# Performance work log

Measured on AMD Instinct MI355X. Metric: run time of the kernel, lower is better.

## Reference

```python
import jax, jax.numpy as jnp
import numpy as np

TOPK = 13
ALPHA = 1.0
BETA = 6.0
NUM_CLASSES = 80
EPS = 1e-9


def _make_boxes(key, shape, max_half):
    # shape = (..., 4): build valid x1y1x2y2 boxes inside a 640x640 image
    kc, ks = jax.random.split(key)
    centers = jax.random.uniform(kc, shape[:-1] + (2,), minval=30.0, maxval=610.0)
    halves = jax.random.uniform(ks, shape[:-1] + (2,), minval=2.0, maxval=max_half)
    return jnp.concatenate([centers - halves, centers + halves], axis=-1)


def setup_inputs() -> dict:
    key = jax.random.key(0)
    k1, k2, k3, k4, k5 = jax.random.split(key, 5)
    B, L, C, n = 16, 8400, NUM_CLASSES, 128
    pred_scores = jax.random.uniform(k1, (B, L, C), dtype=jnp.float32)
    pred_bboxes = _make_boxes(k2, (B, L, 4), 60.0)
    anchor_points = jax.random.uniform(k3, (L, 2), minval=0.0, maxval=640.0)
    gt_labels = jax.random.randint(k4, (B, n), 0, C, dtype=jnp.int32)
    gt_bboxes = _make_boxes(k5, (B, n, 4), 120.0)
    pad_gt_mask = jnp.ones((B, n, 1), dtype=jnp.float32)
    return {"pred_scores": pred_scores, "pred_bboxes": pred_bboxes,
            "anchor_points": anchor_points, "gt_labels": gt_labels,
            "gt_bboxes": gt_bboxes, "pad_gt_mask": pad_gt_mask}


def _batch_iou(box1, box2, eps=1e-9):
    # box1: [B, n, 4], box2: [B, L, 4] -> iou [B, n, L]
    b1 = box1[:, :, None]  # [B,n,1,4]
    b2 = box2[:, None]     # [B,1,L,4]
    x1y1 = jnp.maximum(b1[..., 0:2], b2[..., 0:2])
    x2y2 = jnp.minimum(b1[..., 2:4], b2[..., 2:4])
    overlap = jnp.prod(jnp.clip(x2y2 - x1y1, 0.0), axis=-1)
    area1 = jnp.prod(jnp.clip(b1[..., 2:4] - b1[..., 0:2], 0.0), axis=-1)
    area2 = jnp.prod(jnp.clip(b2[..., 2:4] - b2[..., 0:2], 0.0), axis=-1)
    return overlap / (area1 + area2 - overlap + eps)


def _points_in_bboxes(points, bboxes, eps=EPS):
    # points: [L,2], bboxes: [B,n,4] -> [B,n,L] float
    x = points[None, None, :, 0]
    y = points[None, None, :, 1]
    xmin = bboxes[..., 0:1]; ymin = bboxes[..., 1:2]
    xmax = bboxes[..., 2:3]; ymax = bboxes[..., 3:4]
    l = x - xmin; t = y - ymin; r = xmax - x; b = ymax - y
    d = jnp.minimum(jnp.minimum(l, t), jnp.minimum(r, b))
    return (d > eps).astype(bboxes.dtype)


def _gather_topk(metrics, topk, topk_mask):
    # metrics: [B,n,L] -> one-hot membership of per-gt topk anchors [B,n,L]
    L = metrics.shape[-1]
    _, topk_idxs = jax.lax.top_k(metrics, topk)          # [B,n,topk]
    is_in_topk = jax.nn.one_hot(topk_idxs, L, dtype=metrics.dtype).sum(-2)
    return is_in_topk * topk_mask


def reference(pred_scores, pred_bboxes, anchor_points, gt_labels, gt_bboxes, pad_gt_mask):
    B, n, _ = gt_bboxes.shape
    L = pred_bboxes.shape[1]
    # pairwise IoU between gts and predicted boxes: [B,n,L]
    ious = _batch_iou(gt_bboxes, pred_bboxes)
    # per-gt class scores gathered from pred_scores: [B,n,L]
    scores_cl = jnp.transpose(pred_scores, (0, 2, 1))                 # [B,C,L]
    bbox_cls_scores = jnp.take_along_axis(scores_cl, gt_labels[:, :, None].astype(jnp.int32), axis=1)
    # task-aligned metric
    alignment = (bbox_cls_scores ** ALPHA) * (ious ** BETA)
    is_in_gts = _points_in_bboxes(anchor_points, gt_bboxes)           # [B,n,L]
    is_in_topk = _gather_topk(alignment * is_in_gts, TOPK, pad_gt_mask)
    mask_positive = is_in_topk * is_in_gts * pad_gt_mask              # [B,n,L]
    # resolve anchors assigned to multiple gts: keep max-IoU gt
    mask_pos_sum = mask_positive.sum(-2)                              # [B,L]
    is_max_iou = jnp.transpose(jax.nn.one_hot(jnp.argmax(ious, axis=-2), n, dtype=ious.dtype), (0, 2, 1))
    mask_positive = jnp.where((mask_pos_sum[:, None, :] > 1), is_max_iou, mask_positive)
    mask_pos_sum = mask_positive.sum(-2)
    # assignment
    assigned_gt_index = jnp.argmax(mask_positive, axis=-2)            # [B,L]
    flat_idx = assigned_gt_index + jnp.arange(B, dtype=assigned_gt_index.dtype)[:, None] * n
    assigned_labels = jnp.reshape(gt_labels, (-1,))[flat_idx]
    assigned_labels = jnp.where(mask_pos_sum > 0, assigned_labels, NUM_CLASSES)
    assigned_bboxes = jnp.reshape(gt_bboxes, (-1, 4))[flat_idx]       # [B,L,4]
    assigned_scores = jax.nn.one_hot(assigned_labels, NUM_CLASSES + 1, dtype=pred_scores.dtype)[..., :NUM_CLASSES]
    # rescale scores by normalized alignment metric
    align_m = alignment * mask_positive
    max_metric = align_m.max(-1, keepdims=True)                       # [B,n,1]
    max_iou = (ious * mask_positive).max(-1, keepdims=True)           # [B,n,1]
    align_m = (align_m / (max_metric + EPS)) * max_iou
    assigned_scores = assigned_scores * align_m.max(-2)[..., None]    # [B,L,C]
    return assigned_labels, assigned_bboxes, assigned_scores
```

## Files before the change

kernel.cpp:

```cpp
#include <hip/hip_runtime.h>
#include <stdint.h>

#define BB   16
#define NGT  128
#define LL   8400
#define CC   80
#define KTOP 13
#define SEGW 2112
#define FEPS 1e-9f

typedef float vfloat4 __attribute__((ext_vector_type(4)));

__device__ __forceinline__ float iou_f(float4 g, float4 p) {
    float ix0 = fmaxf(g.x, p.x);
    float iy0 = fmaxf(g.y, p.y);
    float ix1 = fminf(g.z, p.z);
    float iy1 = fminf(g.w, p.w);
    float ow = fmaxf(ix1 - ix0, 0.0f);
    float oh = fmaxf(iy1 - iy0, 0.0f);
    float ov = ow * oh;
    float a1 = fmaxf(g.z - g.x, 0.0f) * fmaxf(g.w - g.y, 0.0f);
    float a2 = fmaxf(p.z - p.x, 0.0f) * fmaxf(p.w - p.y, 0.0f);
    return ov / (a1 + a2 - ov + FEPS);
}

__global__ __launch_bounds__(256) void topk_kernel(
    const float*  __restrict__ pred_scores,
    const float4* __restrict__ pred_bboxes,
    const float2* __restrict__ anchors,
    const int*    __restrict__ gt_labels,
    const float4* __restrict__ gt_bboxes,
    int* __restrict__ claim_count,
    int* __restrict__ claimant)
{
    int wave = threadIdx.x >> 6;
    int lane = threadIdx.x & 63;
    int row  = blockIdx.x;
    int b    = row >> 7;
    int i_gt = row & (NGT - 1);

    float4 g  = gt_bboxes[row];
    int label = gt_labels[row];
    const float*  sc = pred_scores + (size_t)b * LL * CC + label;
    const float4* pb = pred_bboxes + (size_t)b * LL;

    __shared__ unsigned long long wkeys[4 * KTOP];
    __shared__ int s_pick[KTOP];

    int seg  = wave * SEGW;
    int jend = (seg + SEGW < LL) ? seg + SEGW : LL;
    unsigned long long m0 = 0ull;
#pragma unroll 4
    for (int it = 0; it < 33; ++it) {
        int j = seg + (it << 6) + lane;
        if (j < jend) {
            float2 ap = anchors[j];
            float d = fminf(fminf(ap.x - g.x, ap.y - g.y),
                            fminf(g.z - ap.x, g.w - ap.y));
            m0 |= ((unsigned long long)(d > FEPS)) << it;
        }
    }

    unsigned long long keys[KTOP];
#pragma unroll
    for (int k = 0; k < KTOP; ++k) keys[k] = 0ull;

    if (wave == 0 && !(m0 & 1ull)) keys[0] = (unsigned)(~(unsigned)lane);

    {
        unsigned long long mask = m0;
        while (mask) {
            int p = __ffsll(mask) - 1;
            mask &= mask - 1ull;
            int j = seg + (p << 6) + lane;
            float4 pbx = pb[j];
            float iou = iou_f(g, pbx);
            unsigned long long key = (unsigned)(~(unsigned)j);
            if (iou > 0.0f) {
                float s  = sc[(size_t)j * CC];
                float i2 = iou * iou;
                key |= ((unsigned long long)__float_as_uint(s * (i2 * i2 * i2)) << 32);
            }
            if (key > keys[KTOP - 1]) {
                keys[KTOP - 1] = key;
#pragma unroll
                for (int k = KTOP - 1; k > 0; --k) {
                    unsigned long long a = keys[k - 1], c2 = keys[k];
                    keys[k - 1] = (c2 > a) ? c2 : a;
                    keys[k]     = (c2 > a) ? a : c2;
                }
            }
        }
    }

    for (int r = 0; r < KTOP; ++r) {
        unsigned long long head = keys[0];
        unsigned long long m = head;
#pragma unroll
        for (int off = 1; off < 64; off <<= 1) {
            unsigned long long o = __shfl_xor(m, off, 64);
            if (o > m) m = o;
        }
        if (head == m && m != 0ull) {
#pragma unroll
            for (int k = 0; k < KTOP - 1; ++k) keys[k] = keys[k + 1];
            keys[KTOP - 1] = 0ull;
        }
        if (lane == 0) wkeys[wave * KTOP + r] = m;
    }
    __syncthreads();

    if (wave == 0) {
        unsigned long long k1 = (lane < 4 * KTOP) ? wkeys[lane] : 0ull;
        for (int r = 0; r < KTOP; ++r) {
            unsigned long long m = k1;
#pragma unroll
            for (int off = 1; off < 64; off <<= 1) {
                unsigned long long o = __shfl_xor(m, off, 64);
                if (o > m) m = o;
            }
            if (k1 == m && m != 0ull) k1 = 0ull;
            if (lane == 0) s_pick[r] = (int)(~(unsigned)(m & 0xFFFFFFFFull));
        }
    }
    __syncthreads();

    if (threadIdx.x < KTOP) {
        int j = s_pick[threadIdx.x];
        float2 ap = anchors[j];
        float d = fminf(fminf(ap.x - g.x, ap.y - g.y),
                        fminf(g.z - ap.x, g.w - ap.y));
        if (d > FEPS) {
            atomicAdd(claim_count + b * LL + j, 1);
            atomicMax(claimant + b * LL + j, i_gt);
        }
    }
}

__global__ __launch_bounds__(256) void resolve_kernel(
    const float*  __restrict__ pred_scores,
    const float4* __restrict__ pred_bboxes,
    const int*    __restrict__ gt_labels,
    const float4* __restrict__ gt_bboxes,
    const int*    __restrict__ claim_count,
    const int*    __restrict__ claimant,
    int*      __restrict__ assigned_gt,
    float*    __restrict__ align_anchor,
    unsigned* __restrict__ max_metric,
    unsigned* __restrict__ max_iou,
    float*    __restrict__ out_labels,
    float4*   __restrict__ out_bboxes)
{
    int b = blockIdx.y;
    int j = blockIdx.x * 256 + threadIdx.x;

    __shared__ float4 gbox[NGT];
    __shared__ int    glab[NGT];
    if (threadIdx.x < NGT) {
        gbox[threadIdx.x] = gt_bboxes[b * NGT + threadIdx.x];
        glab[threadIdx.x] = gt_labels[b * NGT + threadIdx.x];
    }
    __syncthreads();
    if (j >= LL) return;

    int idx = b * LL + j;
    int cnt = claim_count[idx];
    int g = -1;
    float4 p = pred_bboxes[(size_t)b * LL + j];

    if (cnt == 1) {
        g = claimant[idx];
    } else if (cnt > 1) {
        float best = -1.0f;
        int   bi   = 0;
        for (int i = 0; i < NGT; ++i) {
            float iou = iou_f(gbox[i], p);
            if (iou > best) { best = iou; bi = i; }
        }
        g = bi;
    }
    assigned_gt[idx] = g;

    int label; float4 bb;
    if (g >= 0) {
        float iou = iou_f(gbox[g], p);
        float s   = pred_scores[((size_t)b * LL + j) * CC + glab[g]];
        float i2  = iou * iou;
        float al  = s * (i2 * i2 * i2);
        align_anchor[idx] = al;
        atomicMax(max_metric + b * NGT + g, __float_as_uint(al));
        atomicMax(max_iou    + b * NGT + g, __float_as_uint(iou));
        label = glab[g];
        bb    = gbox[g];
    } else {
        label = CC;
        bb    = gbox[0];
    }
    out_labels[idx] = (float)label;
    out_bboxes[idx] = bb;
}

__global__ __launch_bounds__(256) void score_kernel(
    const int*    __restrict__ gt_labels,
    const int*    __restrict__ assigned_gt,
    const float*  __restrict__ align_anchor,
    const unsigned* __restrict__ max_metric,
    const unsigned* __restrict__ max_iou,
    float*  __restrict__ out_scores)
{
    int t = blockIdx.x * 256 + threadIdx.x;
    __shared__ int   s_lab[256];
    __shared__ float s_f[256];

    int b = t / LL;
    int g = assigned_gt[t];
    int label = CC;
    float f = 0.0f;
    if (g >= 0) {
        label = gt_labels[b * NGT + g];
        float mm = __uint_as_float(max_metric[b * NGT + g]);
        float mi = __uint_as_float(max_iou[b * NGT + g]);
        f = align_anchor[t] / (mm + FEPS) * mi;
    }
    s_lab[threadIdx.x] = label;
    s_f[threadIdx.x]   = f;
    __syncthreads();

    vfloat4* outs = (vfloat4*)(out_scores + (size_t)blockIdx.x * 256 * CC);
    for (int i = threadIdx.x; i < 256 * CC / 4; i += 256) {
        int anchor = i / (CC / 4);
        int c4     = i % (CC / 4);
        int lab    = s_lab[anchor];
        vfloat4 v = {0.f, 0.f, 0.f, 0.f};
        int rel = lab - c4 * 4;
        if (rel >= 0 && rel < 4) v[rel] = s_f[anchor];
        __builtin_nontemporal_store(v, outs + i);
    }
}

extern "C" void kernel_launch(void* const* d_in, const int* in_sizes, int n_in,
                              void* d_out, int out_size, void* d_ws, size_t ws_size,
                              hipStream_t stream)
{
    const float*  pred_scores = (const float*)d_in[0];
    const float4* pred_bboxes = (const float4*)d_in[1];
    const float2* anchors     = (const float2*)d_in[2];
    const int*    gt_labels   = (const int*)d_in[3];
    const float4* gt_bboxes   = (const float4*)d_in[4];

    char* w = (char*)d_ws;
    int*      claim_count  = (int*)(w);
    int*      claimant     = (int*)(w + 537600);
    unsigned* max_metric   = (unsigned*)(w + 1075200);
    unsigned* max_iou      = (unsigned*)(w + 1083392);
    int*      assigned_gt  = (int*)(w + 1091584);
    float*    align_anchor = (float*)(w + 1629184);

    float*  out        = (float*)d_out;
    float*  out_labels = out;
    float4* out_bboxes = (float4*)(out + (size_t)BB * LL);
    float*  out_scores = out + (size_t)BB * LL * 5;

    (void)hipMemsetAsync(w, 0, 1091584, stream);

    topk_kernel<<<BB * NGT, 256, 0, stream>>>(
        pred_scores, pred_bboxes, anchors, gt_labels, gt_bboxes,
        claim_count, claimant);

    dim3 gridC((LL + 255) / 256, BB);
    resolve_kernel<<<gridC, 256, 0, stream>>>(
        pred_scores, pred_bboxes, gt_labels, gt_bboxes,
        claim_count, claimant, assigned_gt, align_anchor, max_metric, max_iou,
        out_labels, out_bboxes);

    score_kernel<<<(BB * LL) / 256, 256, 0, stream>>>(
        gt_labels, assigned_gt, align_anchor, max_metric, max_iou, out_scores);
}
```

Before: 98.45 us.

## Run per-GT topk with a single wave and vectorized anchor loads

The top-k kernel now uses one 64-lane wave per GT row instead of four waves with shared-memory merging. Each lane loads two anchors per float4 load and builds two inside-box bitmasks, with a tail handled separately. The cross-wave reduction through shared memory and its two barriers are gone, and the final winner is held in a register per lane. In exchange each block does four times the serial work per lane and gets less parallelism per GT, relying on the 2048 blocks to fill the GPU.

```diff
diff --git a/kernel.cpp b/kernel.cpp
--- a/kernel.cpp
+++ b/kernel.cpp
@@ -6,7 +6,6 @@
 #define LL   8400
 #define CC   80
 #define KTOP 13
-#define SEGW 2112
 #define FEPS 1e-9f
 
 typedef float vfloat4 __attribute__((ext_vector_type(4)));
@@ -24,7 +23,7 @@
     return ov / (a1 + a2 - ov + FEPS);
 }
 
-__global__ __launch_bounds__(256) void topk_kernel(
+__global__ __launch_bounds__(64) void topk_kernel(
     const float*  __restrict__ pred_scores,
     const float4* __restrict__ pred_bboxes,
     const float2* __restrict__ anchors,
@@ -33,66 +32,97 @@
     int* __restrict__ claim_count,
     int* __restrict__ claimant)
 {
-    int wave = threadIdx.x >> 6;
-    int lane = threadIdx.x & 63;
+    int lane = threadIdx.x;
     int row  = blockIdx.x;
     int b    = row >> 7;
     int i_gt = row & (NGT - 1);
 
     float4 g  = gt_bboxes[row];
     int label = gt_labels[row];
-    const float*  sc = pred_scores + (size_t)b * LL * CC + label;
-    const float4* pb = pred_bboxes + (size_t)b * LL;
-
-    __shared__ unsigned long long wkeys[4 * KTOP];
-    __shared__ int s_pick[KTOP];
-
-    int seg  = wave * SEGW;
-    int jend = (seg + SEGW < LL) ? seg + SEGW : LL;
-    unsigned long long m0 = 0ull;
-#pragma unroll 4
-    for (int it = 0; it < 33; ++it) {
-        int j = seg + (it << 6) + lane;
-        if (j < jend) {
-            float2 ap = anchors[j];
-            float d = fminf(fminf(ap.x - g.x, ap.y - g.y),
-                            fminf(g.z - ap.x, g.w - ap.y));
-            m0 |= ((unsigned long long)(d > FEPS)) << it;
-        }
-    }
+    const float*   sc = pred_scores + (size_t)b * LL * CC + label;
+    const float4*  pb = pred_bboxes + (size_t)b * LL;
+    const vfloat4* a4 = (const vfloat4*)anchors;
 
     unsigned long long keys[KTOP];
 #pragma unroll
     for (int k = 0; k < KTOP; ++k) keys[k] = 0ull;
 
-    if (wave == 0 && !(m0 & 1ull)) keys[0] = (unsigned)(~(unsigned)lane);
-
+    auto insert = [&](unsigned long long key) {
+        if (key > keys[KTOP - 1]) {
+            keys[KTOP - 1] = key;
+#pragma unroll
+            for (int k = KTOP - 1; k > 0; --k) {
+                unsigned long long a = keys[k - 1], c2 = keys[k];
+                keys[k - 1] = (c2 > a) ? c2 : a;
+                keys[k]     = (c2 > a) ? a : c2;
+            }
+        }
+    };
+    auto eval_insert = [&](int j) {
+        float4 pbx = pb[j];
+        float iou = iou_f(g, pbx);
+        unsigned long long key = (unsigned)(~(unsigned)j);
+        if (iou > 0.0f) {
+            float s  = sc[(size_t)j * CC];
+            float i2 = iou * iou;
+            key |= ((unsigned long long)__float_as_uint(s * (i2 * i2 * i2)) << 32);
+        }
+        insert(key);
+    };
+
+    unsigned long long mA = 0ull, mB = 0ull;
+    for (int b8 = 0; b8 < 8; ++b8) {
+        vfloat4 v[8];
+#pragma unroll
+        for (int u = 0; u < 8; ++u)
+            v[u] = a4[lane + ((b8 * 8 + u) << 6)];
+#pragma unroll
+        for (int u = 0; u < 8; ++u) {
+            int t = b8 * 8 + u;
+            float dA = fminf(fminf(v[u].x - g.x, v[u].y - g.y),
+                             fminf(g.z - v[u].x, g.w - v[u].y));
+            float dB = fminf(fminf(v[u].z - g.x, v[u].w - g.y),
+                             fminf(g.z - v[u].z, g.w - v[u].w));
+            mA |= ((unsigned long long)(dA > FEPS)) << t;
+            mB |= ((unsigned long long)(dB > FEPS)) << t;
+        }
+    }
     {
-        unsigned long long mask = m0;
-        while (mask) {
-            int p = __ffsll(mask) - 1;
-            mask &= mask - 1ull;
-            int j = seg + (p << 6) + lane;
-            float4 pbx = pb[j];
-            float iou = iou_f(g, pbx);
-            unsigned long long key = (unsigned)(~(unsigned)j);
-            if (iou > 0.0f) {
-                float s  = sc[(size_t)j * CC];
-                float i2 = iou * iou;
-                key |= ((unsigned long long)__float_as_uint(s * (i2 * i2 * i2)) << 32);
-            }
-            if (key > keys[KTOP - 1]) {
-                keys[KTOP - 1] = key;
-#pragma unroll
-                for (int k = KTOP - 1; k > 0; --k) {
-                    unsigned long long a = keys[k - 1], c2 = keys[k];
-                    keys[k - 1] = (c2 > a) ? c2 : a;
-                    keys[k]     = (c2 > a) ? a : c2;
-                }
-            }
-        }
-    }
-
+        vfloat4 v0 = a4[4096 + lane];
+        float dA = fminf(fminf(v0.x - g.x, v0.y - g.y),
+                         fminf(g.z - v0.x, g.w - v0.y));
+        float dB = fminf(fminf(v0.z - g.x, v0.w - g.y),
+                         fminf(g.z - v0.z, g.w - v0.w));
+        int f = 4096 + lane;
+        if (dA > FEPS) eval_insert(2 * f);
+        if (dB > FEPS) eval_insert(2 * f + 1);
+        if (lane < 40) {
+            vfloat4 v1 = a4[4160 + lane];
+            float eA = fminf(fminf(v1.x - g.x, v1.y - g.y),
+                             fminf(g.z - v1.x, g.w - v1.y));
+            float eB = fminf(fminf(v1.z - g.x, v1.w - g.y),
+                             fminf(g.z - v1.z, g.w - v1.w));
+            int f1 = 4160 + lane;
+            if (eA > FEPS) eval_insert(2 * f1);
+            if (eB > FEPS) eval_insert(2 * f1 + 1);
+        }
+    }
+
+    if (lane < KTOP) {
+        if (!(mA & 1ull)) insert((unsigned long long)(unsigned)(~(unsigned)(2 * lane)));
+        if (!(mB & 1ull)) insert((unsigned long long)(unsigned)(~(unsigned)(2 * lane + 1)));
+    }
+
+    while (mA) {
+        int t = __ffsll(mA) - 1; mA &= mA - 1ull;
+        eval_insert(2 * (lane + (t << 6)));
+    }
+    while (mB) {
+        int t = __ffsll(mB) - 1; mB &= mB - 1ull;
+        eval_insert(2 * (lane + (t << 6)) + 1);
+    }
+
+    unsigned long long winner = 0ull;
     for (int r = 0; r < KTOP; ++r) {
         unsigned long long head = keys[0];
         unsigned long long m = head;
@@ -106,27 +136,11 @@
             for (int k = 0; k < KTOP - 1; ++k) keys[k] = keys[k + 1];
             keys[KTOP - 1] = 0ull;
         }
-        if (lane == 0) wkeys[wave * KTOP + r] = m;
-    }
-    __syncthreads();
-
-    if (wave == 0) {
-        unsigned long long k1 = (lane < 4 * KTOP) ? wkeys[lane] : 0ull;
-        for (int r = 0; r < KTOP; ++r) {
-            unsigned long long m = k1;
-#pragma unroll
-            for (int off = 1; off < 64; off <<= 1) {
-                unsigned long long o = __shfl_xor(m, off, 64);
-                if (o > m) m = o;
-            }
-            if (k1 == m && m != 0ull) k1 = 0ull;
-            if (lane == 0) s_pick[r] = (int)(~(unsigned)(m & 0xFFFFFFFFull));
-        }
-    }
-    __syncthreads();
-
-    if (threadIdx.x < KTOP) {
-        int j = s_pick[threadIdx.x];
+        if (lane == r) winner = m;
+    }
+
+    if (lane < KTOP && winner != 0ull) {
+        int j = (int)(~(unsigned)(winner & 0xFFFFFFFFull));
         float2 ap = anchors[j];
         float d = fminf(fminf(ap.x - g.x, ap.y - g.y),
                         fminf(g.z - ap.x, g.w - ap.y));
@@ -263,7 +277,7 @@
 
     (void)hipMemsetAsync(w, 0, 1091584, stream);
 
-    topk_kernel<<<BB * NGT, 256, 0, stream>>>(
+    topk_kernel<<<BB * NGT, 64, 0, stream>>>(
         pred_scores, pred_bboxes, anchors, gt_labels, gt_bboxes,
         claim_count, claimant);
 
```

Result: faster. 92.96 us (-5.6%).

## Split top-k into anchor-parallel candidate compaction and per-gt selection

Applied to the files above, without the earlier changes.

Replaces the per-gt block that scanned all 8400 anchors with an anchor-parallel kernel. That kernel tests each anchor against all 128 gts from shared memory and appends positive-metric candidates into per-gt record lists via atomics. A single-wave select kernel then runs top-13 over only those candidates and fills remaining slots with zero-metric anchors in index order, keeping a full-scan fallback for overflow or a small workspace. This aims to cut the redundant per-gt scanning and block-level reductions, at the cost of global atomics, an extra launch and a larger workspace.

```diff
diff --git a/kernel.cpp b/kernel.cpp
--- a/kernel.cpp
+++ b/kernel.cpp
@@ -6,7 +6,7 @@
 #define LL   8400
 #define CC   80
 #define KTOP 13
-#define SEGW 2112
+#define CAP  1024
 #define FEPS 1e-9f
 
 typedef float vfloat4 __attribute__((ext_vector_type(4)));
@@ -24,77 +24,112 @@
     return ov / (a1 + a2 - ov + FEPS);
 }
 
-__global__ __launch_bounds__(256) void topk_kernel(
+#define SORT2(a,b) { unsigned long long _t=(a), _u=(b); (a)=(_u>_t)?_u:_t; (b)=(_u>_t)?_t:_u; }
+#define INSERT13(key) do { unsigned long long _k=(key); if (_k > k12) { k12=_k; \
+    SORT2(k11,k12) SORT2(k10,k11) SORT2(k9,k10) SORT2(k8,k9) SORT2(k7,k8) \
+    SORT2(k6,k7)  SORT2(k5,k6)  SORT2(k4,k5) SORT2(k3,k4) SORT2(k2,k3) \
+    SORT2(k1,k2)  SORT2(k0,k1) } } while(0)
+#define POP13() { k0=k1;k1=k2;k2=k3;k3=k4;k4=k5;k5=k6;k6=k7;k7=k8;k8=k9;k9=k10;k10=k11;k11=k12;k12=0ull; }
+
+__global__ __launch_bounds__(256) void cand_kernel(
     const float*  __restrict__ pred_scores,
     const float4* __restrict__ pred_bboxes,
     const float2* __restrict__ anchors,
     const int*    __restrict__ gt_labels,
     const float4* __restrict__ gt_bboxes,
+    unsigned long long* __restrict__ records,
+    int* __restrict__ cand_cnt)
+{
+    int b = blockIdx.y;
+    int j = blockIdx.x * 256 + threadIdx.x;
+
+    __shared__ float4 gbox[NGT];
+    __shared__ int    glab[NGT];
+    if (threadIdx.x < NGT) {
+        gbox[threadIdx.x] = gt_bboxes[b * NGT + threadIdx.x];
+        glab[threadIdx.x] = gt_labels[b * NGT + threadIdx.x];
+    }
+    __syncthreads();
+    if (j >= LL) return;
+
+    float2 ap = anchors[j];
+    float4 p  = pred_bboxes[(size_t)b * LL + j];
+    const float* srow = pred_scores + ((size_t)b * LL + j) * CC;
+
+    for (int i = 0; i < NGT; ++i) {
+        float4 gg = gbox[i];
+        float d = fminf(fminf(ap.x - gg.x, ap.y - gg.y),
+                        fminf(gg.z - ap.x, gg.w - ap.y));
+        if (d > FEPS) {
+            float iou = iou_f(gg, p);
+            if (iou > 0.0f) {
+                float s  = srow[glab[i]];
+                float i2 = iou * iou;
+                float met = s * (i2 * i2 * i2);
+                if (met > 0.0f) {
+                    int rrow = b * NGT + i;
+                    int slot = atomicAdd(cand_cnt + rrow, 1);
+                    if (slot < CAP)
+                        records[(size_t)rrow * CAP + slot] =
+                            ((unsigned long long)__float_as_uint(met) << 32)
+                            | (unsigned)(~(unsigned)j);
+                }
+            }
+        }
+    }
+}
+
+__global__ __launch_bounds__(64) void select_kernel(
+    const float*  __restrict__ pred_scores,
+    const float4* __restrict__ pred_bboxes,
+    const float2* __restrict__ anchors,
+    const int*    __restrict__ gt_labels,
+    const float4* __restrict__ gt_bboxes,
+    const unsigned long long* __restrict__ records,
+    const int* __restrict__ cand_cnt,
+    int force_fallback,
     int* __restrict__ claim_count,
     int* __restrict__ claimant)
 {
-    int wave = threadIdx.x >> 6;
-    int lane = threadIdx.x & 63;
+    int lane = threadIdx.x;
     int row  = blockIdx.x;
     int b    = row >> 7;
     int i_gt = row & (NGT - 1);
 
-    float4 g  = gt_bboxes[row];
-    int label = gt_labels[row];
-    const float*  sc = pred_scores + (size_t)b * LL * CC + label;
-    const float4* pb = pred_bboxes + (size_t)b * LL;
-
-    __shared__ unsigned long long wkeys[4 * KTOP];
-    __shared__ int s_pick[KTOP];
-
-    int seg  = wave * SEGW;
-    int jend = (seg + SEGW < LL) ? seg + SEGW : LL;
-    unsigned long long m0 = 0ull;
-#pragma unroll 4
-    for (int it = 0; it < 33; ++it) {
-        int j = seg + (it << 6) + lane;
-        if (j < jend) {
+    float4 g = gt_bboxes[row];
+    unsigned long long k0=0,k1=0,k2=0,k3=0,k4=0,k5=0,k6=0,k7=0,k8=0,k9=0,k10=0,k11=0,k12=0;
+
+    int cnt = cand_cnt[row];
+    if (force_fallback || cnt > CAP) {
+        int label = gt_labels[row];
+        const float*  sc = pred_scores + (size_t)b * LL * CC + label;
+        const float4* pb = pred_bboxes + (size_t)b * LL;
+        for (int j = lane; j < LL; j += 64) {
             float2 ap = anchors[j];
             float d = fminf(fminf(ap.x - g.x, ap.y - g.y),
                             fminf(g.z - ap.x, g.w - ap.y));
-            m0 |= ((unsigned long long)(d > FEPS)) << it;
-        }
-    }
-
-    unsigned long long keys[KTOP];
-#pragma unroll
-    for (int k = 0; k < KTOP; ++k) keys[k] = 0ull;
-
-    if (wave == 0 && !(m0 & 1ull)) keys[0] = (unsigned)(~(unsigned)lane);
-
-    {
-        unsigned long long mask = m0;
-        while (mask) {
-            int p = __ffsll(mask) - 1;
-            mask &= mask - 1ull;
-            int j = seg + (p << 6) + lane;
-            float4 pbx = pb[j];
-            float iou = iou_f(g, pbx);
-            unsigned long long key = (unsigned)(~(unsigned)j);
-            if (iou > 0.0f) {
-                float s  = sc[(size_t)j * CC];
-                float i2 = iou * iou;
-                key |= ((unsigned long long)__float_as_uint(s * (i2 * i2 * i2)) << 32);
-            }
-            if (key > keys[KTOP - 1]) {
-                keys[KTOP - 1] = key;
-#pragma unroll
-                for (int k = KTOP - 1; k > 0; --k) {
-                    unsigned long long a = keys[k - 1], c2 = keys[k];
-                    keys[k - 1] = (c2 > a) ? c2 : a;
-                    keys[k]     = (c2 > a) ? a : c2;
+            if (d > FEPS) {
+                float4 p = pb[j];
+                float iou = iou_f(g, p);
+                if (iou > 0.0f) {
+                    float s  = sc[(size_t)j * CC];
+                    float i2 = iou * iou;
+                    float met = s * (i2 * i2 * i2);
+                    if (met > 0.0f)
+                        INSERT13(((unsigned long long)__float_as_uint(met) << 32)
+                                 | (unsigned)(~(unsigned)j));
                 }
             }
         }
-    }
-
+    } else {
+        const unsigned long long* rr = records + (size_t)row * CAP;
+        for (int t = lane; t < cnt; t += 64)
+            INSERT13(rr[t]);
+    }
+
+    unsigned long long winner = 0ull;
     for (int r = 0; r < KTOP; ++r) {
-        unsigned long long head = keys[0];
+        unsigned long long head = k0;
         unsigned long long m = head;
 #pragma unroll
         for (int off = 1; off < 64; off <<= 1) {
@@ -102,37 +137,38 @@
             if (o > m) m = o;
         }
         if (head == m && m != 0ull) {
-#pragma unroll
-            for (int k = 0; k < KTOP - 1; ++k) keys[k] = keys[k + 1];
-            keys[KTOP - 1] = 0ull;
-        }
-        if (lane == 0) wkeys[wave * KTOP + r] = m;
-    }
-    __syncthreads();
-
-    if (wave == 0) {
-        unsigned long long k1 = (lane < 4 * KTOP) ? wkeys[lane] : 0ull;
-        for (int r = 0; r < KTOP; ++r) {
-            unsigned long long m = k1;
-#pragma unroll
-            for (int off = 1; off < 64; off <<= 1) {
-                unsigned long long o = __shfl_xor(m, off, 64);
-                if (o > m) m = o;
-            }
-            if (k1 == m && m != 0ull) k1 = 0ull;
-            if (lane == 0) s_pick[r] = (int)(~(unsigned)(m & 0xFFFFFFFFull));
-        }
-    }
-    __syncthreads();
-
-    if (threadIdx.x < KTOP) {
-        int j = s_pick[threadIdx.x];
-        float2 ap = anchors[j];
+            POP13();
+        }
+        if (lane == r) winner = m;
+    }
+
+    int jwv = -1;
+    if (lane < KTOP && winner != 0ull)
+        jwv = (int)(~(unsigned)(winner & 0xFFFFFFFFull));
+
+    bool marked = false;
+    for (int r = 0; r < KTOP; ++r) {
+        int jv = __shfl(jwv, r, 64);
+        if (jv == lane) marked = true;
+    }
+    unsigned long long nonpos = ~__ballot(marked);
+    int P = __popcll(__ballot(jwv >= 0));
+
+    int base = b * LL;
+    if (jwv >= 0) {
+        atomicAdd(claim_count + base + jwv, 1);
+        atomicMax(claimant + base + jwv, i_gt);
+    }
+    if (lane >= P && lane < KTOP) {
+        unsigned long long mask = nonpos;
+        for (int t = 0; t < lane - P; ++t) mask &= mask - 1ull;
+        int jf = __ffsll(mask) - 1;
+        float2 ap = anchors[jf];
         float d = fminf(fminf(ap.x - g.x, ap.y - g.y),
                         fminf(g.z - ap.x, g.w - ap.y));
         if (d > FEPS) {
-            atomicAdd(claim_count + b * LL + j, 1);
-            atomicMax(claimant + b * LL + j, i_gt);
+            atomicAdd(claim_count + base + jf, 1);
+            atomicMax(claimant + base + jf, i_gt);
         }
     }
 }
@@ -253,19 +289,31 @@
     int*      claimant     = (int*)(w + 537600);
     unsigned* max_metric   = (unsigned*)(w + 1075200);
     unsigned* max_iou      = (unsigned*)(w + 1083392);
-    int*      assigned_gt  = (int*)(w + 1091584);
-    float*    align_anchor = (float*)(w + 1629184);
+    int*      cand_cnt     = (int*)(w + 1091584);
+    int*      assigned_gt  = (int*)(w + 1099776);
+    float*    align_anchor = (float*)(w + 1637376);
+    unsigned long long* records = (unsigned long long*)(w + 2174976);
+
+    const size_t WS_NEEDED = 2174976ull + (size_t)BB * NGT * CAP * 8ull;
+    int force_fallback = (ws_size < WS_NEEDED) ? 1 : 0;
 
     float*  out        = (float*)d_out;
     float*  out_labels = out;
     float4* out_bboxes = (float4*)(out + (size_t)BB * LL);
     float*  out_scores = out + (size_t)BB * LL * 5;
 
-    (void)hipMemsetAsync(w, 0, 1091584, stream);
-
-    topk_kernel<<<BB * NGT, 256, 0, stream>>>(
+    (void)hipMemsetAsync(w, 0, 1099776, stream);
+
+    if (!force_fallback) {
+        dim3 gridG((LL + 255) / 256, BB);
+        cand_kernel<<<gridG, 256, 0, stream>>>(
+            pred_scores, pred_bboxes, anchors, gt_labels, gt_bboxes,
+            records, cand_cnt);
+    }
+
+    select_kernel<<<BB * NGT, 64, 0, stream>>>(
         pred_scores, pred_bboxes, anchors, gt_labels, gt_bboxes,
-        claim_count, claimant);
+        records, cand_cnt, force_fallback, claim_count, claimant);
 
     dim3 gridC((LL + 255) / 256, BB);
     resolve_kernel<<<gridC, 256, 0, stream>>>(
```

After: 118.2 us. 20.1% more time.
